# Kernel tuning notes

Measured on AMD Instinct MI355X. Metric: run time of the kernel, lower is better.

Reference implementation:

```python
import jax, jax.numpy as jnp
import numpy as np

D_MODEL, SEQ, D_HEAD, N_HEAD, D_MLP = 1024, 2048, 64, 16, 4096
BATCH = 2
LN_EPS = 1e-5


def layer_norm(x, gamma, beta):
    mu = jnp.mean(x, axis=-1, keepdims=True)
    var = jnp.mean(jnp.square(x - mu), axis=-1, keepdims=True)
    return (x - mu) * jax.lax.rsqrt(var + LN_EPS) * gamma + beta


def setup_inputs() -> dict:
    key = jax.random.key(0)
    ks = jax.random.split(key, 10)
    s = 1.0 / np.sqrt(D_MODEL)
    x = jax.random.normal(ks[0], (BATCH, SEQ, D_MODEL), dtype=jnp.float32)
    # per-head Q/K/V projections, stacked: [H, d_model, d_head]
    wq = jax.random.uniform(ks[1], (N_HEAD, D_MODEL, D_HEAD), jnp.float32, -s, s)
    wk = jax.random.uniform(ks[2], (N_HEAD, D_MODEL, D_HEAD), jnp.float32, -s, s)
    wv = jax.random.uniform(ks[3], (N_HEAD, D_MODEL, D_HEAD), jnp.float32, -s, s)
    wo = jax.random.uniform(ks[4], (N_HEAD * D_HEAD, D_MODEL), jnp.float32, -s, s)
    sm = 1.0 / np.sqrt(D_MLP)
    w_in = jax.random.uniform(ks[5], (D_MODEL, D_MLP), jnp.float32, -s, s)
    b_in = jax.random.uniform(ks[6], (D_MLP,), jnp.float32, -s, s)
    w_out = jax.random.uniform(ks[7], (D_MLP, D_MODEL), jnp.float32, -sm, sm)
    b_out = jax.random.uniform(ks[8], (D_MODEL,), jnp.float32, -sm, sm)
    g1 = jnp.ones((D_MODEL,), jnp.float32)
    bt1 = jnp.zeros((D_MODEL,), jnp.float32)
    g2 = jnp.ones((D_MODEL,), jnp.float32)
    bt2 = jnp.zeros((D_MODEL,), jnp.float32)
    return {"x": x, "wq": wq, "wk": wk, "wv": wv, "wo": wo,
            "w_in": w_in, "b_in": b_in, "w_out": w_out, "b_out": b_out,
            "g1": g1, "bt1": bt1, "g2": g2, "bt2": bt2}


def reference(x, wq, wk, wv, wo, w_in, b_in, w_out, b_out, g1, bt1, g2, bt2):
    B, S, D = x.shape
    # multi-head attention (all heads batched)
    q = jnp.einsum('bsd,hde->bhse', x, wq)  # [B,H,S,dh]
    k = jnp.einsum('bsd,hde->bhse', x, wk)
    v = jnp.einsum('bsd,hde->bhse', x, wv)
    scores = jnp.einsum('bhie,bhje->bhij', q, k) / np.sqrt(D_HEAD)
    causal = jnp.tril(jnp.ones((S, S), dtype=bool))
    scores = jnp.where(causal, scores, -jnp.inf)
    attn = jax.nn.softmax(scores, axis=-1)
    head_out = jnp.einsum('bhij,bhje->bhie', attn, v)  # [B,H,S,dh]
    # concat heads in order (head 0 first) -> [B,S,H*dh]
    head_out = jnp.transpose(head_out, (0, 2, 1, 3)).reshape(B, S, N_HEAD * D_HEAD)
    x = x + layer_norm(head_out @ wo, g1, bt1)
    mlp = jax.nn.relu(x @ w_in + b_in) @ w_out + b_out
    x = x + layer_norm(mlp, g2, bt2)
    return x
```

## Files before the change

kernel.cpp:

```cpp
#include <hip/hip_runtime.h>
#include <hip/hip_bf16.h>
#include <math.h>

#define DM 1024
#define SEQ 2048
#define DH 64
#define NH 16
#define DMLP 4096
#define BATCH 2
#define ROWS (BATCH*SEQ)

typedef __attribute__((ext_vector_type(4))) float f32x4;
typedef __attribute__((ext_vector_type(8))) short bf16x8;
typedef __attribute__((ext_vector_type(4))) unsigned int u32x4;

__device__ __forceinline__ void gl2lds16(const __hip_bfloat16* g, __hip_bfloat16* l) {
  __builtin_amdgcn_global_load_lds(
      (const __attribute__((address_space(1))) void*)g,
      (__attribute__((address_space(3))) void*)l, 16, 0, 0);
}

__device__ __forceinline__ float bfu2f(unsigned short u) {
  union { unsigned int i; float f; } cvt;
  cvt.i = ((unsigned int)u) << 16;
  return cvt.f;
}

__device__ __forceinline__ unsigned short f2bu(float f) {
  __hip_bfloat16 h = __float2bfloat16(f);
  return *reinterpret_cast<unsigned short*>(&h);
}

template<int K, int OUT_BF16, int BIAS, int RELU>
__global__ __launch_bounds__(512) void gemm256(
    const __hip_bfloat16* __restrict__ A,
    const __hip_bfloat16* __restrict__ BT,
    float* __restrict__ Cf,
    __hip_bfloat16* __restrict__ Cb,
    const float* __restrict__ bias,
    int N)
{
  constexpr int NT = K / 64;
  __shared__ __align__(16) __hip_bfloat16 As[2][16384];
  __shared__ __align__(16) __hip_bfloat16 Bs[2][16384];
  const int t    = threadIdx.x;
  const int wave = t >> 6;
  const int lane = t & 63;
  const int col  = lane & 15;
  const int quad = lane >> 4;
  const int m0 = blockIdx.x * 256;
  const int n0 = blockIdx.y * 256;
  const int wm = (wave >> 2) * 128;
  const int wn = (wave & 3) * 64;

  const int tr = t >> 3;
  const int tc = (t & 7) ^ (tr & 7);
  const __hip_bfloat16* gA = A  + (size_t)(m0 + tr) * K + tc * 8;
  const __hip_bfloat16* gB = BT + (size_t)(n0 + tr) * K + tc * 8;

  const int sw  = col & 7;
  const int ao0 = ((quad)     ^ sw) * 8;
  const int ao1 = ((4 + quad) ^ sw) * 8;

  f32x4 acc[8][4] = {};

#define STAGE_A(h, u) do {                                                     \
    gl2lds16(gA + (size_t)(h)*128*K + (u)*64,                                  \
             &As[(u)&1][(h)*8192 + wave*512]);                                 \
    gl2lds16(gA + (size_t)(h)*128*K + (u)*64 + (size_t)64*K,                   \
             &As[(u)&1][(h)*8192 + 4096 + wave*512]);                          \
  } while (0)
#define STAGE_B(h, u) do {                                                     \
    gl2lds16(gB + (size_t)(h)*128*K + (u)*64,                                  \
             &Bs[(u)&1][(h)*8192 + wave*512]);                                 \
    gl2lds16(gB + (size_t)(h)*128*K + (u)*64 + (size_t)64*K,                   \
             &Bs[(u)&1][(h)*8192 + 4096 + wave*512]);                          \
  } while (0)
#define LOAD_A(base) do { _Pragma("unroll")                                    \
    for (int i = 0; i < 4; ++i) {                                              \
      af[i][0] = *(const bf16x8*)(pA + (base) + i*1024 + ao0);                 \
      af[i][1] = *(const bf16x8*)(pA + (base) + i*1024 + ao1);                 \
    } } while (0)
#define LOAD_BX(arr, base) do { _Pragma("unroll")                              \
    for (int j = 0; j < 2; ++j) {                                              \
      arr[j][0] = *(const bf16x8*)(pB + (base) + j*1024 + ao0);                \
      arr[j][1] = *(const bf16x8*)(pB + (base) + j*1024 + ao1);                \
    } } while (0)
#define PHASE_TAIL(MB, NB, BARR) do {                                          \
    asm volatile("s_barrier" ::: "memory");                                    \
    asm volatile("s_waitcnt lgkmcnt(0)" ::: "memory");                         \
    __builtin_amdgcn_s_setprio(1);                                             \
    _Pragma("unroll")                                                          \
    for (int kk = 0; kk < 2; ++kk)                                             \
      _Pragma("unroll")                                                        \
      for (int i = 0; i < 4; ++i)                                              \
        _Pragma("unroll")                                                      \
        for (int j = 0; j < 2; ++j)                                            \
          acc[(MB)+i][(NB)+j] = __builtin_amdgcn_mfma_f32_16x16x32_bf16(       \
              af[i][kk], BARR[j][kk], acc[(MB)+i][(NB)+j], 0, 0, 0);           \
    __builtin_amdgcn_s_setprio(0);                                             \
    asm volatile("s_barrier" ::: "memory");                                    \
  } while (0)

  STAGE_A(0, 0); STAGE_B(0, 0); STAGE_A(1, 0); STAGE_B(1, 0);
  if (NT > 1) {
    STAGE_A(0, 1); STAGE_B(0, 1); STAGE_A(1, 1); STAGE_B(1, 1);
    asm volatile("s_waitcnt vmcnt(8)" ::: "memory");
  } else {
    asm volatile("s_waitcnt vmcnt(0)" ::: "memory");
  }
  asm volatile("s_barrier" ::: "memory");

  #pragma unroll 2
  for (int u = 0; u < NT; ++u) {
    const __hip_bfloat16* pA = As[u & 1] + (wm + col) * 64;
    const __hip_bfloat16* pB = Bs[u & 1] + (wn + col) * 64;
    const bool s2 = (u + 2 < NT);
    bf16x8 af[4][2], bl[2][2], bh[2][2];

    LOAD_A(0);
    LOAD_BX(bl, 0);
    PHASE_TAIL(0, 0, bl);

    LOAD_BX(bh, 2048);
    PHASE_TAIL(0, 2, bh);

    LOAD_A(4096);
    if (s2) { STAGE_B(0, u + 2); STAGE_B(1, u + 2); }
    PHASE_TAIL(4, 2, bh);

    if (s2) {
      STAGE_A(0, u + 2); STAGE_A(1, u + 2);
      asm volatile("s_waitcnt vmcnt(8)" ::: "memory");
    } else {
      asm volatile("s_waitcnt vmcnt(0)" ::: "memory");
    }
    PHASE_TAIL(4, 0, bl);
  }
#undef STAGE_A
#undef STAGE_B
#undef LOAD_A
#undef LOAD_BX
#undef PHASE_TAIL

  #pragma unroll
  for (int mi = 0; mi < 8; ++mi) {
    #pragma unroll
    for (int ni = 0; ni < 4; ++ni) {
      const int cn = n0 + wn + ni*16 + col;
      float bv = 0.f;
      if (BIAS) bv = bias[cn];
      #pragma unroll
      for (int r = 0; r < 4; ++r) {
        const int cm = m0 + wm + mi*16 + quad*4 + r;
        float v = acc[mi][ni][r];
        if (BIAS) v += bv;
        if (RELU) v = fmaxf(v, 0.f);
        if (OUT_BF16) Cb[(size_t)cm * N + cn] = __float2bfloat16(v);
        else          Cf[(size_t)cm * N + cn] = v;
      }
    }
  }
}

template<int KS>
__global__ __launch_bounds__(256) void gemm128(
    const __hip_bfloat16* __restrict__ A,
    const __hip_bfloat16* __restrict__ BT,
    float* __restrict__ Cf,
    int N, int K, long long zstride)
{
  constexpr int NT = KS / 64;
  static_assert(NT >= 2, "pipeline needs >=2 K-tiles");
  __shared__ __align__(16) __hip_bfloat16 As[2][8192];
  __shared__ __align__(16) __hip_bfloat16 Bs[2][8192];
  const int t    = threadIdx.x;
  const int wave = t >> 6;
  const int lane = t & 63;
  const int col  = lane & 15;
  const int quad = lane >> 4;
  const int m0 = blockIdx.x * 128;
  const int n0 = blockIdx.y * 128;
  const int kz = (int)blockIdx.z * KS;
  const int wm = (wave >> 1) * 64;
  const int wn = (wave & 1) * 64;

  const int tr = t >> 3;
  const int tc = (t & 7) ^ (tr & 7);
  const __hip_bfloat16* gA = A  + (size_t)(m0 + tr) * K + kz + tc * 8;
  const __hip_bfloat16* gB = BT + (size_t)(n0 + tr) * K + kz + tc * 8;

  const int sw  = col & 7;
  const int ao0 = ((quad)     ^ sw) * 8;
  const int ao1 = ((4 + quad) ^ sw) * 8;

  f32x4 acc[4][4] = {};

#define SA(u) do { _Pragma("unroll")                                           \
    for (int q = 0; q < 4; ++q)                                                \
      gl2lds16(gA + (size_t)(q*32)*K + (u)*64,                                 \
               &As[(u)&1][q*2048 + wave*512]);                                 \
  } while (0)
#define SB(u) do { _Pragma("unroll")                                           \
    for (int q = 0; q < 4; ++q)                                                \
      gl2lds16(gB + (size_t)(q*32)*K + (u)*64,                                 \
               &Bs[(u)&1][q*2048 + wave*512]);                                 \
  } while (0)

  SA(0); SB(0); SA(1);

  #pragma unroll 2
  for (int v = 0; v < NT; ++v) {
    const __hip_bfloat16* pA = As[v & 1] + (wm + col) * 64;
    const __hip_bfloat16* pB = Bs[v & 1] + (wn + col) * 64;
    bf16x8 af[4][2], bf[4][2];

    if (v + 1 < NT) {
      SB(v + 1);
      asm volatile("s_waitcnt vmcnt(8)" ::: "memory");
    } else {
      asm volatile("s_waitcnt vmcnt(0)" ::: "memory");
    }
    asm volatile("s_barrier" ::: "memory");
    #pragma unroll
    for (int i = 0; i < 4; ++i) {
      af[i][0] = *(const bf16x8*)(pA + i*1024 + ao0);
      af[i][1] = *(const bf16x8*)(pA + i*1024 + ao1);
    }
    #pragma unroll
    for (int j = 0; j < 2; ++j) {
      bf[j][0] = *(const bf16x8*)(pB + j*1024 + ao0);
      bf[j][1] = *(const bf16x8*)(pB + j*1024 + ao1);
    }
    asm volatile("s_waitcnt lgkmcnt(0)" ::: "memory");
    __builtin_amdgcn_s_setprio(1);
    #pragma unroll
    for (int kk = 0; kk < 2; ++kk)
      #pragma unroll
      for (int i = 0; i < 4; ++i)
        #pragma unroll
        for (int j = 0; j < 2; ++j)
          acc[i][j] = __builtin_amdgcn_mfma_f32_16x16x32_bf16(
              af[i][kk], bf[j][kk], acc[i][j], 0, 0, 0);
    __builtin_amdgcn_s_setprio(0);
    asm volatile("s_barrier" ::: "memory");

    if (v + 2 < NT) SA(v + 2);
    #pragma unroll
    for (int j = 2; j < 4; ++j) {
      bf[j][0] = *(const bf16x8*)(pB + j*1024 + ao0);
      bf[j][1] = *(const bf16x8*)(pB + j*1024 + ao1);
    }
    asm volatile("s_waitcnt lgkmcnt(0)" ::: "memory");
    __builtin_amdgcn_s_setprio(1);
    #pragma unroll
    for (int kk = 0; kk < 2; ++kk)
      #pragma unroll
      for (int i = 0; i < 4; ++i)
        #pragma unroll
        for (int j = 2; j < 4; ++j)
          acc[i][j] = __builtin_amdgcn_mfma_f32_16x16x32_bf16(
              af[i][kk], bf[j][kk], acc[i][j], 0, 0, 0);
    __builtin_amdgcn_s_setprio(0);
    asm volatile("s_barrier" ::: "memory");
  }
#undef SA
#undef SB

  float* Co = Cf + (size_t)blockIdx.z * zstride;
  #pragma unroll
  for (int i = 0; i < 4; ++i) {
    #pragma unroll
    for (int j = 0; j < 4; ++j) {
      const int cn = n0 + wn + j*16 + col;
      #pragma unroll
      for (int r = 0; r < 4; ++r) {
        const int cm = m0 + wm + i*16 + quad*4 + r;
        Co[(size_t)cm * N + cn] = acc[i][j][r];
      }
    }
  }
}

__global__ __launch_bounds__(256) void attn_kernel(
    const __hip_bfloat16* __restrict__ qkv,
    const __hip_bfloat16* __restrict__ vt,
    __hip_bfloat16* __restrict__ aout,
    __hip_bfloat16* __restrict__ opart,
    float* __restrict__ lpart)
{
  __shared__ __align__(16) __hip_bfloat16 Ks[2][64*64];
  __shared__ __align__(16) __hip_bfloat16 Vts[2][64*64];

  const int bh = blockIdx.x, b = bh >> 4, h = bh & 15;
  const int t = threadIdx.x, wave = t >> 6, lane = t & 63;
  const int col = lane & 15, quad = lane >> 4;
  const float SC = 0.125f * 1.44269504f;

  const int r0  = t >> 3;
  const int cs0 = (t & 7) ^ (r0 & 7);
  const int pk0 = ((r0 >> 4) & 1)*32 + ((r0 >> 2) & 3)*8 + (r0 & 3);
  const __hip_bfloat16* kbase = qkv + (size_t)b*SEQ*3072 + 1024 + h*64;
  const __hip_bfloat16* vbase = vt + (size_t)bh*64*SEQ;

#define KISSUE(j0, buf) do {                                                      \
    gl2lds16(kbase + (size_t)((j0) + pk0    )*3072 + cs0*8, &Ks[buf][wave*512]);  \
    gl2lds16(kbase + (size_t)((j0) + pk0 + 4)*3072 + cs0*8, &Ks[buf][2048 + wave*512]); \
  } while (0)
#define VISSUE(j0, buf) do {                                                      \
    gl2lds16(vbase + (size_t)r0*SEQ        + (j0) + cs0*8,  &Vts[buf][wave*512]); \
    gl2lds16(vbase + (size_t)(32 + r0)*SEQ + (j0) + cs0*8,  &Vts[buf][2048 + wave*512]); \
  } while (0)

  const int y = (int)blockIdx.y;
  int c, tl;
  if (y < 16)      { c = 0; tl = 15 - y; }
  else if (y < 28) { c = 1; tl = 31 - y; }
  else if (y < 36) { c = 2; tl = 43 - y; }
  else             { c = 3; tl = 51 - y; }
  const int jbeg = c * 8;
  const int njt  = 2*tl + 2;
  const int jend = min(jbeg + 8, njt);

  const int i0 = tl * 128;
  const int iw = i0 + wave*32;

  bf16x8 aq[2][2];
  #pragma unroll
  for (int ib = 0; ib < 2; ib++)
    #pragma unroll
    for (int kk = 0; kk < 2; kk++)
      aq[ib][kk] = *(const bf16x8*)&qkv[((size_t)(b*SEQ + iw + ib*16 + col))*3072 + h*64 + kk*32 + quad*8];

  f32x4 O[4][2] = {};
  float lsum[2] = {0.f, 0.f};

  KISSUE(jbeg * 64, 0);
  VISSUE(jbeg * 64, 0);
  for (int jt = jbeg; jt < jend; jt++) {
    const int cur = (jt - jbeg) & 1;
    const int j0 = jt * 64;
    const bool pf = (jt + 1 < jend);
    asm volatile("s_barrier" ::: "memory");
    if (pf) {
      KISSUE(j0 + 64, cur ^ 1);
      VISSUE(j0 + 64, cur ^ 1);
      asm volatile("s_waitcnt vmcnt(4)" ::: "memory");
    } else {
      asm volatile("s_waitcnt vmcnt(0)" ::: "memory");
    }

    f32x4 S[4][2] = {};
    __builtin_amdgcn_s_setprio(1);
    #pragma unroll
    for (int kk = 0; kk < 2; kk++) {
      const int sl = ((kk*4 + quad) ^ (col & 7)) * 8;
      #pragma unroll
      for (int jl = 0; jl < 4; jl++) {
        bf16x8 bk = *(const bf16x8*)&Ks[cur][(jl*16 + col)*64 + sl];
        #pragma unroll
        for (int ib = 0; ib < 2; ib++)
          S[jl][ib] = __builtin_amdgcn_mfma_f32_16x16x32_bf16(bk, aq[ib][kk], S[jl][ib], 0, 0, 0);
      }
    }
    __builtin_amdgcn_s_setprio(0);

    unsigned int pw[2][4][2];
    #pragma unroll
    for (int ib = 0; ib < 2; ib++) {
      const int ig = iw + ib*16 + col;
      if (j0 + 64 > iw + ib*16) {
        #pragma unroll
        for (int jl = 0; jl < 4; jl++) {
          const int jb = j0 + (jl & 1)*32 + quad*8 + (jl >> 1)*4;
          float p[4];
          #pragma unroll
          for (int r = 0; r < 4; r++) {
            float v = __builtin_amdgcn_exp2f(S[jl][ib][r] * SC);
            if (jb + r > ig) v = 0.f;
            p[r] = v;
            lsum[ib] += v;
          }
          pw[ib][jl][0] = (unsigned int)f2bu(p[0]) | ((unsigned int)f2bu(p[1]) << 16);
          pw[ib][jl][1] = (unsigned int)f2bu(p[2]) | ((unsigned int)f2bu(p[3]) << 16);
        }
      } else {
        #pragma unroll
        for (int jl = 0; jl < 4; jl++) {
          float p[4];
          #pragma unroll
          for (int r = 0; r < 4; r++) {
            p[r] = __builtin_amdgcn_exp2f(S[jl][ib][r] * SC);
            lsum[ib] += p[r];
          }
          pw[ib][jl][0] = (unsigned int)f2bu(p[0]) | ((unsigned int)f2bu(p[1]) << 16);
          pw[ib][jl][1] = (unsigned int)f2bu(p[2]) | ((unsigned int)f2bu(p[3]) << 16);
        }
      }
    }

    __builtin_amdgcn_s_setprio(1);
    #pragma unroll
    for (int kk = 0; kk < 2; kk++) {
      const int sl = ((kk*4 + quad) ^ (col & 7)) * 8;
      bf16x8 ap[2];
      #pragma unroll
      for (int ib = 0; ib < 2; ib++) {
        u32x4 bu = { pw[ib][kk][0], pw[ib][kk][1], pw[ib][kk+2][0], pw[ib][kk+2][1] };
        ap[ib] = __builtin_bit_cast(bf16x8, bu);
      }
      #pragma unroll
      for (int et = 0; et < 4; et++) {
        bf16x8 bv = *(const bf16x8*)&Vts[cur][(et*16 + col)*64 + sl];
        #pragma unroll
        for (int ib = 0; ib < 2; ib++)
          O[et][ib] = __builtin_amdgcn_mfma_f32_16x16x32_bf16(bv, ap[ib], O[et][ib], 0, 0, 0);
      }
    }
    __builtin_amdgcn_s_setprio(0);
  }

  #pragma unroll
  for (int ib = 0; ib < 2; ib++) {
    float s = lsum[ib];
    s += __shfl_xor(s, 16);
    s += __shfl_xor(s, 32);
    const int m = b*SEQ + iw + ib*16 + col;
    if (tl < 4) {
      const float inv = __builtin_amdgcn_rcpf(s);
      #pragma unroll
      for (int et = 0; et < 4; et++) {
        ushort4 o = { f2bu(O[et][ib][0]*inv), f2bu(O[et][ib][1]*inv),
                      f2bu(O[et][ib][2]*inv), f2bu(O[et][ib][3]*inv) };
        *(ushort4*)&aout[(size_t)m*DM + h*64 + et*16 + quad*4] = o;
      }
    } else {
      __hip_bfloat16* op = opart + ((size_t)c*ROWS + m)*DM + h*64;
      #pragma unroll
      for (int et = 0; et < 4; et++) {
        ushort4 o = { f2bu(O[et][ib][0]), f2bu(O[et][ib][1]),
                      f2bu(O[et][ib][2]), f2bu(O[et][ib][3]) };
        *(ushort4*)&op[et*16 + quad*4] = o;
      }
      if (quad == 0) lpart[((size_t)c*ROWS + m)*16 + h] = s;
    }
  }
#undef KISSUE
#undef VISSUE
}

__global__ __launch_bounds__(256) void attn_finalize(
    const __hip_bfloat16* __restrict__ opart,
    const float* __restrict__ lpart,
    __hip_bfloat16* __restrict__ aout)
{
  const int y = blockIdx.x;
  const int b = y / 1536;
  const int rem = y % 1536;
  const int tl = 4 + (rem >> 7);
  const int rr = rem & 127;
  const int m = b*SEQ + tl*128 + rr;
  const int nch = (tl >> 2) + 1;
  const int tid = threadIdx.x;
  const int h = tid >> 4;
  float o0 = 0.f, o1 = 0.f, o2 = 0.f, o3 = 0.f, l = 0.f;
  for (int c = 0; c < nch; ++c) {
    const ushort4 v = ((const ushort4*)(opart + ((size_t)c*ROWS + m)*DM))[tid];
    o0 += bfu2f(v.x); o1 += bfu2f(v.y); o2 += bfu2f(v.z); o3 += bfu2f(v.w);
    l  += lpart[((size_t)c*ROWS + m)*16 + h];
  }
  const float inv = __builtin_amdgcn_rcpf(l);
  __hip_bfloat16* p = aout + (size_t)m*DM + tid*4;
  p[0] = __float2bfloat16(o0 * inv);
  p[1] = __float2bfloat16(o1 * inv);
  p[2] = __float2bfloat16(o2 * inv);
  p[3] = __float2bfloat16(o3 * inv);
}

__global__ __launch_bounds__(256) void ln_res(
    const float* __restrict__ y0,
    const float* __restrict__ y1,
    const float* __restrict__ bias,
    const float* __restrict__ xres,
    float* __restrict__ xout,
    __hip_bfloat16* __restrict__ bout,
    const float* __restrict__ gamma,
    const float* __restrict__ beta)
{
  const int row = blockIdx.x;
  const int t = threadIdx.x;
  float4 v = ((const float4*)(y0 + (size_t)row*DM))[t];
  if (y1) {
    const float4 w = ((const float4*)(y1 + (size_t)row*DM))[t];
    v.x += w.x; v.y += w.y; v.z += w.z; v.w += w.w;
  }
  if (bias) {
    const float4 w = ((const float4*)bias)[t];
    v.x += w.x; v.y += w.y; v.z += w.z; v.w += w.w;
  }
  float s  = v.x + v.y + v.z + v.w;
  float sq = v.x*v.x + v.y*v.y + v.z*v.z + v.w*v.w;
  #pragma unroll
  for (int off = 32; off > 0; off >>= 1) {
    s  += __shfl_down(s, off);
    sq += __shfl_down(sq, off);
  }
  __shared__ float red[8];
  const int wave = t >> 6, lane = t & 63;
  if (lane == 0) { red[wave] = s; red[4 + wave] = sq; }
  __syncthreads();
  s  = red[0] + red[1] + red[2] + red[3];
  sq = red[4] + red[5] + red[6] + red[7];
  const float mu   = s * (1.f/DM);
  const float var  = sq * (1.f/DM) - mu*mu;
  const float rstd = rsqrtf(var + 1e-5f);
  const float4 g  = ((const float4*)gamma)[t];
  const float4 bt = ((const float4*)beta)[t];
  const float4 xr = ((const float4*)(xres + (size_t)row*DM))[t];
  float4 o;
  o.x = (v.x - mu)*rstd*g.x + bt.x + xr.x;
  o.y = (v.y - mu)*rstd*g.y + bt.y + xr.y;
  o.z = (v.z - mu)*rstd*g.z + bt.z + xr.z;
  o.w = (v.w - mu)*rstd*g.w + bt.w + xr.w;
  ((float4*)(xout + (size_t)row*DM))[t] = o;
  if (bout) {
    __hip_bfloat16* bp = bout + (size_t)row*DM + t*4;
    bp[0] = __float2bfloat16(o.x);
    bp[1] = __float2bfloat16(o.y);
    bp[2] = __float2bfloat16(o.z);
    bp[3] = __float2bfloat16(o.w);
  }
}

__global__ __launch_bounds__(256) void transpose_cvt(
    const float* __restrict__ src, __hip_bfloat16* __restrict__ dst,
    int K, int N, long long sz, long long dz)
{
  __shared__ float tile[32][33];
  const int z = blockIdx.z;
  const int k0 = blockIdx.y * 32, n0 = blockIdx.x * 32;
  const int tx = threadIdx.x & 31, ty = threadIdx.x >> 5;
  const float* s = src + (size_t)z*sz;
  __hip_bfloat16* d = dst + (size_t)z*dz;
  for (int i = ty; i < 32; i += 8)
    tile[i][tx] = s[(size_t)(k0+i)*N + n0 + tx];
  __syncthreads();
  for (int i = ty; i < 32; i += 8)
    d[(size_t)(n0+i)*K + k0 + tx] = __float2bfloat16(tile[tx][i]);
}

__global__ __launch_bounds__(256) void transpose_v(
    const __hip_bfloat16* __restrict__ qkv, __hip_bfloat16* __restrict__ vt)
{
  __shared__ __hip_bfloat16 tile[32][33];
  const int bh = blockIdx.z, b = bh >> 4, h = bh & 15;
  const int s0 = blockIdx.x * 32, e0 = blockIdx.y * 32;
  const int tx = threadIdx.x & 31, ty = threadIdx.x >> 5;
  for (int i = ty; i < 32; i += 8)
    tile[i][tx] = qkv[(size_t)(b*SEQ + s0+i)*3072 + 2048 + h*64 + e0 + tx];
  __syncthreads();
  for (int i = ty; i < 32; i += 8)
    vt[((size_t)bh*64 + e0+i)*SEQ + s0 + tx] = tile[tx][i];
}

__global__ __launch_bounds__(256) void cvt_bf16(
    const float* __restrict__ src, __hip_bfloat16* __restrict__ dst, int n4)
{
  const int i = blockIdx.x*256 + threadIdx.x;
  if (i < n4) {
    const float4 v = ((const float4*)src)[i];
    dst[i*4+0] = __float2bfloat16(v.x);
    dst[i*4+1] = __float2bfloat16(v.y);
    dst[i*4+2] = __float2bfloat16(v.z);
    dst[i*4+3] = __float2bfloat16(v.w);
  }
}

extern "C" void kernel_launch(void* const* d_in, const int* in_sizes, int n_in,
                              void* d_out, int out_size, void* d_ws, size_t ws_size,
                              hipStream_t stream)
{
  const float* x     = (const float*)d_in[0];
  const float* wq    = (const float*)d_in[1];
  const float* wk    = (const float*)d_in[2];
  const float* wv    = (const float*)d_in[3];
  const float* wo    = (const float*)d_in[4];
  const float* w_in  = (const float*)d_in[5];
  const float* b_in  = (const float*)d_in[6];
  const float* w_out = (const float*)d_in[7];
  const float* b_out = (const float*)d_in[8];
  const float* g1    = (const float*)d_in[9];
  const float* bt1   = (const float*)d_in[10];
  const float* g2    = (const float*)d_in[11];
  const float* bt2   = (const float*)d_in[12];
  float* out = (float*)d_out;

  char* ws = (char*)d_ws;
  __hip_bfloat16* xb     = (__hip_bfloat16*)(ws + 0);
  __hip_bfloat16* wqkvT  = (__hip_bfloat16*)(ws + 8388608);
  __hip_bfloat16* woT    = (__hip_bfloat16*)(ws + 14680064);
  __hip_bfloat16* w_inT  = (__hip_bfloat16*)(ws + 16777216);
  __hip_bfloat16* w_outT = (__hip_bfloat16*)(ws + 25165824);
  __hip_bfloat16* qkvb   = (__hip_bfloat16*)(ws + 33554432);
  __hip_bfloat16* vtb    = (__hip_bfloat16*)(ws + 58720256);
  __hip_bfloat16* attn_o = (__hip_bfloat16*)(ws + 0);
  __hip_bfloat16* opart  = (__hip_bfloat16*)(ws + 67108864);
  float*          lpart  = (float*)(ws + 100663296);
  float*          P0     = (float*)(ws + 33554432);
  float*          x1     = (float*)(ws + 75497472);
  __hip_bfloat16* x1b    = (__hip_bfloat16*)(ws + 92274688);
  __hip_bfloat16* hbuf   = (__hip_bfloat16*)(ws + 33554432);
  float*          M0     = (float*)(ws + 0);
  float*          M1     = (float*)(ws + 100663296);
  float*          P1     = (float*)(ws + 50331648);

  const long long PROJ_ZS = (long long)ROWS * DM;
  const long long MLP_ZS  = 100663296LL / 4;

  cvt_bf16<<<ROWS*DM/4/256, 256, 0, stream>>>(x, xb, ROWS*DM/4);

  transpose_cvt<<<dim3(2,32,16), 256, 0, stream>>>(wq, wqkvT,             DM, DH, (long long)DM*DH, (long long)DH*DM);
  transpose_cvt<<<dim3(2,32,16), 256, 0, stream>>>(wk, wqkvT + 1024*1024, DM, DH, (long long)DM*DH, (long long)DH*DM);
  transpose_cvt<<<dim3(2,32,16), 256, 0, stream>>>(wv, wqkvT + 2048*1024, DM, DH, (long long)DM*DH, (long long)DH*DM);
  transpose_cvt<<<dim3(32,32,1),  256, 0, stream>>>(wo,    woT,    DM,   DM,   0, 0);
  transpose_cvt<<<dim3(128,32,1), 256, 0, stream>>>(w_in,  w_inT,  DM,   DMLP, 0, 0);
  transpose_cvt<<<dim3(32,128,1), 256, 0, stream>>>(w_out, w_outT, DMLP, DM,   0, 0);

  gemm256<DM,1,0,0><<<dim3(ROWS/256, 3072/256), 512, 0, stream>>>(xb, wqkvT, nullptr, qkvb, nullptr, 3072);
  transpose_v<<<dim3(SEQ/32, 2, BATCH*NH), 256, 0, stream>>>(qkvb, vtb);
  attn_kernel<<<dim3(BATCH*NH, 40), 256, 0, stream>>>(qkvb, vtb, attn_o, opart, lpart);
  attn_finalize<<<3072, 256, 0, stream>>>(opart, lpart, attn_o);
  gemm128<512><<<dim3(ROWS/128, DM/128, 2), 256, 0, stream>>>(attn_o, woT, P0, DM, DM, PROJ_ZS);
  ln_res<<<ROWS, 256, 0, stream>>>(P0, P1, nullptr, x, x1, x1b, g1, bt1);
  gemm256<DM,1,1,1><<<dim3(ROWS/256, DMLP/256), 512, 0, stream>>>(x1b, w_inT, nullptr, hbuf, b_in, DMLP);
  gemm128<2048><<<dim3(ROWS/128, DM/128, 2), 256, 0, stream>>>(hbuf, w_outT, M0, DM, DMLP, MLP_ZS);
  ln_res<<<ROWS, 256, 0, stream>>>(M0, M1, b_out, x1, out, nullptr, g2, bt2);
}
```

Baseline: 227.2 us.

## Run MLP down-projection with 256-tile split-K=4 GEMM and bf16 partials

The MLP output GEMM moves from the 128x128 split-K=2 kernel with fp32 partials to the 256x256 kernel with a split-K of four, writing bf16 partials into four workspace slots. A new ln_res4 kernel sums the four bf16 partials plus bias before the layernorm and residual. The three Q/K/V weight transposes are merged into one launch. The aim is better tile reuse, fewer partial-sum bytes written and read, and fewer launches. The cost is bf16 rounding of the partial sums, which lowers accuracy, and a grid of only 256 blocks.

```diff
diff --git a/kernel.cpp b/kernel.cpp
--- a/kernel.cpp
+++ b/kernel.cpp
@@ -31,16 +31,17 @@
   return *reinterpret_cast<unsigned short*>(&h);
 }
 
-template<int K, int OUT_BF16, int BIAS, int RELU>
+template<int K, int KS, int OUT_BF16, int BIAS, int RELU>
 __global__ __launch_bounds__(512) void gemm256(
     const __hip_bfloat16* __restrict__ A,
     const __hip_bfloat16* __restrict__ BT,
     float* __restrict__ Cf,
     __hip_bfloat16* __restrict__ Cb,
     const float* __restrict__ bias,
-    int N)
-{
-  constexpr int NT = K / 64;
+    int N, long long zs1, long long zs2)
+{
+  constexpr int NT = KS / 64;
+  static_assert(NT >= 2, "pipeline needs >=2 K-tiles");
   __shared__ __align__(16) __hip_bfloat16 As[2][16384];
   __shared__ __align__(16) __hip_bfloat16 Bs[2][16384];
   const int t    = threadIdx.x;
@@ -50,13 +51,14 @@
   const int quad = lane >> 4;
   const int m0 = blockIdx.x * 256;
   const int n0 = blockIdx.y * 256;
+  const int kz = (int)blockIdx.z * KS;
   const int wm = (wave >> 2) * 128;
   const int wn = (wave & 3) * 64;
 
   const int tr = t >> 3;
   const int tc = (t & 7) ^ (tr & 7);
-  const __hip_bfloat16* gA = A  + (size_t)(m0 + tr) * K + tc * 8;
-  const __hip_bfloat16* gB = BT + (size_t)(n0 + tr) * K + tc * 8;
+  const __hip_bfloat16* gA = A  + (size_t)(m0 + tr) * K + kz + tc * 8;
+  const __hip_bfloat16* gB = BT + (size_t)(n0 + tr) * K + kz + tc * 8;
 
   const int sw  = col & 7;
   const int ao0 = ((quad)     ^ sw) * 8;
@@ -103,12 +105,8 @@
   } while (0)
 
   STAGE_A(0, 0); STAGE_B(0, 0); STAGE_A(1, 0); STAGE_B(1, 0);
-  if (NT > 1) {
-    STAGE_A(0, 1); STAGE_B(0, 1); STAGE_A(1, 1); STAGE_B(1, 1);
-    asm volatile("s_waitcnt vmcnt(8)" ::: "memory");
-  } else {
-    asm volatile("s_waitcnt vmcnt(0)" ::: "memory");
-  }
+  STAGE_A(0, 1); STAGE_B(0, 1); STAGE_A(1, 1); STAGE_B(1, 1);
+  asm volatile("s_waitcnt vmcnt(8)" ::: "memory");
   asm volatile("s_barrier" ::: "memory");
 
   #pragma unroll 2
@@ -143,6 +141,10 @@
 #undef LOAD_BX
 #undef PHASE_TAIL
 
+  const size_t zoff = (size_t)(blockIdx.z & 1) * (size_t)zs1
+                    + (size_t)(blockIdx.z >> 1) * (size_t)zs2;
+  __hip_bfloat16* Cbz = Cb + zoff;
+  float*          Cfz = Cf + zoff;
   #pragma unroll
   for (int mi = 0; mi < 8; ++mi) {
     #pragma unroll
@@ -156,18 +158,20 @@
         float v = acc[mi][ni][r];
         if (BIAS) v += bv;
         if (RELU) v = fmaxf(v, 0.f);
-        if (OUT_BF16) Cb[(size_t)cm * N + cn] = __float2bfloat16(v);
-        else          Cf[(size_t)cm * N + cn] = v;
+        if (OUT_BF16) Cbz[(size_t)cm * N + cn] = __float2bfloat16(v);
+        else          Cfz[(size_t)cm * N + cn] = v;
       }
     }
   }
 }
 
-template<int KS>
+template<int KS, int SPLIT, int OUT_BF16, int BIAS, int RELU>
 __global__ __launch_bounds__(256) void gemm128(
     const __hip_bfloat16* __restrict__ A,
     const __hip_bfloat16* __restrict__ BT,
     float* __restrict__ Cf,
+    __hip_bfloat16* __restrict__ Cb,
+    const float* __restrict__ bias,
     int N, int K, long long zstride)
 {
   constexpr int NT = KS / 64;
@@ -181,7 +185,7 @@
   const int quad = lane >> 4;
   const int m0 = blockIdx.x * 128;
   const int n0 = blockIdx.y * 128;
-  const int kz = (int)blockIdx.z * KS;
+  const int kz = (SPLIT > 1) ? (int)blockIdx.z * KS : 0;
   const int wm = (wave >> 1) * 64;
   const int wn = (wave & 1) * 64;
 
@@ -267,16 +271,22 @@
 #undef SA
 #undef SB
 
-  float* Co = Cf + (size_t)blockIdx.z * zstride;
+  float* Cfz = (SPLIT > 1) ? (Cf + (size_t)blockIdx.z * zstride) : Cf;
   #pragma unroll
   for (int i = 0; i < 4; ++i) {
     #pragma unroll
     for (int j = 0; j < 4; ++j) {
       const int cn = n0 + wn + j*16 + col;
+      float bv = 0.f;
+      if (BIAS) bv = bias[cn];
       #pragma unroll
       for (int r = 0; r < 4; ++r) {
         const int cm = m0 + wm + i*16 + quad*4 + r;
-        Co[(size_t)cm * N + cn] = acc[i][j][r];
+        float v = acc[i][j][r];
+        if (BIAS) v += bv;
+        if (RELU) v = fmaxf(v, 0.f);
+        if (OUT_BF16) Cb[(size_t)cm * N + cn] = __float2bfloat16(v);
+        else          Cfz[(size_t)cm * N + cn] = v;
       }
     }
   }
@@ -532,6 +542,57 @@
   }
 }
 
+__global__ __launch_bounds__(256) void ln_res4(
+    const __hip_bfloat16* __restrict__ y0,
+    const __hip_bfloat16* __restrict__ y1,
+    const __hip_bfloat16* __restrict__ y2,
+    const __hip_bfloat16* __restrict__ y3,
+    const float* __restrict__ bias,
+    const float* __restrict__ xres,
+    float* __restrict__ xout,
+    const float* __restrict__ gamma,
+    const float* __restrict__ beta)
+{
+  const int row = blockIdx.x;
+  const int t = threadIdx.x;
+  const size_t off = (size_t)row*DM;
+  const ushort4 a = ((const ushort4*)(y0 + off))[t];
+  const ushort4 b = ((const ushort4*)(y1 + off))[t];
+  const ushort4 cc = ((const ushort4*)(y2 + off))[t];
+  const ushort4 d = ((const ushort4*)(y3 + off))[t];
+  const float4 bv = ((const float4*)bias)[t];
+  float4 v;
+  v.x = bfu2f(a.x) + bfu2f(b.x) + bfu2f(cc.x) + bfu2f(d.x) + bv.x;
+  v.y = bfu2f(a.y) + bfu2f(b.y) + bfu2f(cc.y) + bfu2f(d.y) + bv.y;
+  v.z = bfu2f(a.z) + bfu2f(b.z) + bfu2f(cc.z) + bfu2f(d.z) + bv.z;
+  v.w = bfu2f(a.w) + bfu2f(b.w) + bfu2f(cc.w) + bfu2f(d.w) + bv.w;
+  float s  = v.x + v.y + v.z + v.w;
+  float sq = v.x*v.x + v.y*v.y + v.z*v.z + v.w*v.w;
+  #pragma unroll
+  for (int o = 32; o > 0; o >>= 1) {
+    s  += __shfl_down(s, o);
+    sq += __shfl_down(sq, o);
+  }
+  __shared__ float red[8];
+  const int wave = t >> 6, lane = t & 63;
+  if (lane == 0) { red[wave] = s; red[4 + wave] = sq; }
+  __syncthreads();
+  s  = red[0] + red[1] + red[2] + red[3];
+  sq = red[4] + red[5] + red[6] + red[7];
+  const float mu   = s * (1.f/DM);
+  const float var  = sq * (1.f/DM) - mu*mu;
+  const float rstd = rsqrtf(var + 1e-5f);
+  const float4 g  = ((const float4*)gamma)[t];
+  const float4 bt = ((const float4*)beta)[t];
+  const float4 xr = ((const float4*)(xres + off))[t];
+  float4 o;
+  o.x = (v.x - mu)*rstd*g.x + bt.x + xr.x;
+  o.y = (v.y - mu)*rstd*g.y + bt.y + xr.y;
+  o.z = (v.z - mu)*rstd*g.z + bt.z + xr.z;
+  o.w = (v.w - mu)*rstd*g.w + bt.w + xr.w;
+  ((float4*)(xout + off))[t] = o;
+}
+
 __global__ __launch_bounds__(256) void transpose_cvt(
     const float* __restrict__ src, __hip_bfloat16* __restrict__ dst,
     int K, int N, long long sz, long long dz)
@@ -547,6 +608,24 @@
   __syncthreads();
   for (int i = ty; i < 32; i += 8)
     d[(size_t)(n0+i)*K + k0 + tx] = __float2bfloat16(tile[tx][i]);
+}
+
+__global__ __launch_bounds__(256) void transpose_wqkv(
+    const float* __restrict__ wq, const float* __restrict__ wk,
+    const float* __restrict__ wv, __hip_bfloat16* __restrict__ dst)
+{
+  __shared__ float tile[32][33];
+  const int z = blockIdx.z, op = z >> 4, hh = z & 15;
+  const float* srcs[3] = { wq, wk, wv };
+  const float* s = srcs[op] + (size_t)hh * DM * DH;
+  __hip_bfloat16* d = dst + (size_t)z * DH * DM;
+  const int k0 = blockIdx.y * 32, n0 = blockIdx.x * 32;
+  const int tx = threadIdx.x & 31, ty = threadIdx.x >> 5;
+  for (int i = ty; i < 32; i += 8)
+    tile[i][tx] = s[(size_t)(k0+i)*DH + n0 + tx];
+  __syncthreads();
+  for (int i = ty; i < 32; i += 8)
+    d[(size_t)(n0+i)*DM + k0 + tx] = __float2bfloat16(tile[tx][i]);
 }
 
 __global__ __launch_bounds__(256) void transpose_v(
@@ -607,32 +686,33 @@
   __hip_bfloat16* opart  = (__hip_bfloat16*)(ws + 67108864);
   float*          lpart  = (float*)(ws + 100663296);
   float*          P0     = (float*)(ws + 33554432);
+  float*          P1     = (float*)(ws + 50331648);
   float*          x1     = (float*)(ws + 75497472);
   __hip_bfloat16* x1b    = (__hip_bfloat16*)(ws + 92274688);
   __hip_bfloat16* hbuf   = (__hip_bfloat16*)(ws + 33554432);
-  float*          M0     = (float*)(ws + 0);
-  float*          M1     = (float*)(ws + 100663296);
-  float*          P1     = (float*)(ws + 50331648);
+  __hip_bfloat16* mp0    = (__hip_bfloat16*)(ws + 0);
+  __hip_bfloat16* mp1    = (__hip_bfloat16*)(ws + 8388608);
+  __hip_bfloat16* mp2    = (__hip_bfloat16*)(ws + 92274688);
+  __hip_bfloat16* mp3    = (__hip_bfloat16*)(ws + 100663296);
 
   const long long PROJ_ZS = (long long)ROWS * DM;
-  const long long MLP_ZS  = 100663296LL / 4;
+  const long long MZS1 = 8388608LL / 2;
+  const long long MZS2 = 92274688LL / 2;
 
   cvt_bf16<<<ROWS*DM/4/256, 256, 0, stream>>>(x, xb, ROWS*DM/4);
 
-  transpose_cvt<<<dim3(2,32,16), 256, 0, stream>>>(wq, wqkvT,             DM, DH, (long long)DM*DH, (long long)DH*DM);
-  transpose_cvt<<<dim3(2,32,16), 256, 0, stream>>>(wk, wqkvT + 1024*1024, DM, DH, (long long)DM*DH, (long long)DH*DM);
-  transpose_cvt<<<dim3(2,32,16), 256, 0, stream>>>(wv, wqkvT + 2048*1024, DM, DH, (long long)DM*DH, (long long)DH*DM);
+  transpose_wqkv<<<dim3(2,32,48), 256, 0, stream>>>(wq, wk, wv, wqkvT);
   transpose_cvt<<<dim3(32,32,1),  256, 0, stream>>>(wo,    woT,    DM,   DM,   0, 0);
   transpose_cvt<<<dim3(128,32,1), 256, 0, stream>>>(w_in,  w_inT,  DM,   DMLP, 0, 0);
   transpose_cvt<<<dim3(32,128,1), 256, 0, stream>>>(w_out, w_outT, DMLP, DM,   0, 0);
 
-  gemm256<DM,1,0,0><<<dim3(ROWS/256, 3072/256), 512, 0, stream>>>(xb, wqkvT, nullptr, qkvb, nullptr, 3072);
+  gemm256<DM,DM,1,0,0><<<dim3(ROWS/256, 3072/256, 1), 512, 0, stream>>>(xb, wqkvT, nullptr, qkvb, nullptr, 3072, 0, 0);
   transpose_v<<<dim3(SEQ/32, 2, BATCH*NH), 256, 0, stream>>>(qkvb, vtb);
   attn_kernel<<<dim3(BATCH*NH, 40), 256, 0, stream>>>(qkvb, vtb, attn_o, opart, lpart);
   attn_finalize<<<3072, 256, 0, stream>>>(opart, lpart, attn_o);
-  gemm128<512><<<dim3(ROWS/128, DM/128, 2), 256, 0, stream>>>(attn_o, woT, P0, DM, DM, PROJ_ZS);
+  gemm128<512,2,0,0,0><<<dim3(ROWS/128, DM/128, 2), 256, 0, stream>>>(attn_o, woT, P0, nullptr, nullptr, DM, DM, PROJ_ZS);
   ln_res<<<ROWS, 256, 0, stream>>>(P0, P1, nullptr, x, x1, x1b, g1, bt1);
-  gemm256<DM,1,1,1><<<dim3(ROWS/256, DMLP/256), 512, 0, stream>>>(x1b, w_inT, nullptr, hbuf, b_in, DMLP);
-  gemm128<2048><<<dim3(ROWS/128, DM/128, 2), 256, 0, stream>>>(hbuf, w_outT, M0, DM, DMLP, MLP_ZS);
-  ln_res<<<ROWS, 256, 0, stream>>>(M0, M1, b_out, x1, out, nullptr, g2, bt2);
-}
+  gemm256<DM,DM,1,1,1><<<dim3(ROWS/256, DMLP/256, 1), 512, 0, stream>>>(x1b, w_inT, nullptr, hbuf, b_in, DMLP, 0, 0);
+  gemm256<DMLP,DM,1,0,0><<<dim3(ROWS/256, DM/256, 4), 512, 0, stream>>>(hbuf, w_outT, nullptr, mp0, nullptr, DM, MZS1, MZS2);
+  ln_res4<<<ROWS, 256, 0, stream>>>(mp0, mp1, mp2, mp3, b_out, x1, out, g2, bt2);
+}
```

New measurement: 222.7 us. Within noise of the previous version (-1.9%).
